# Performance work log

Hardware: AMD Instinct MI355X
Metric: run time of the kernel (lower is better)

The kernel has to match this reference:

```python
import jax, jax.numpy as jnp
import numpy as np
import math

B, S, D, H = 2, 2048, 1024, 16
DK = D // H  # 64


def _rope_tables(seq_len, dim):
    # matches RotaryEmbedding: inv_freq over arange(0, dim, 2)/dim
    inv_freq = 1.0 / (10000.0 ** (jnp.arange(0, dim, 2, dtype=jnp.float32) / dim))
    pos = jnp.arange(seq_len, dtype=jnp.float32)
    freqs = pos[:, None] * inv_freq[None, :]  # [S, dim/2]
    return jnp.cos(freqs), jnp.sin(freqs)


def _apply_rope(x, cos, sin):
    # x: [B, S, H, DK]; cos/sin: [S, DK/2] -> broadcast over heads
    cos = cos[:, None, :]
    sin = sin[:, None, :]
    t = x.shape[-1] // 2
    x1, x2 = x[..., :t], x[..., t:]
    return jnp.concatenate([x1 * cos - x2 * sin, x1 * sin + x2 * cos], axis=-1)


def setup_inputs() -> dict:
    key = jax.random.key(0)
    ks = jax.random.split(key, 12)
    sc = 1.0 / math.sqrt(D)
    inp = {
        'q': jax.random.normal(ks[0], (B, S, D), jnp.float32),
        'k': jax.random.normal(ks[1], (B, S, D), jnp.float32),
        'v': jax.random.normal(ks[2], (B, S, D), jnp.float32),
        'mask': jnp.tril(jnp.ones((S, S), jnp.int32))[None, None, :, :],  # causal [1,1,S,S]
        'Wq': jax.random.normal(ks[3], (D, D), jnp.float32) * sc,
        'bq': jnp.zeros((D,), jnp.float32),
        'Wk': jax.random.normal(ks[4], (D, D), jnp.float32) * sc,
        'bk': jnp.zeros((D,), jnp.float32),
        'Wv': jax.random.normal(ks[5], (D, D), jnp.float32) * sc,
        'bv': jnp.zeros((D,), jnp.float32),
        'Wo': jax.random.normal(ks[6], (D, D), jnp.float32) * sc,
        'bo': jnp.zeros((D,), jnp.float32),
    }
    return inp


def reference(q, k, v, mask, Wq, bq, Wk, bk, Wv, bv, Wo, bo):
    b, sq, _ = q.shape
    sk = k.shape[1]
    # QKV projections (torch Linear: x @ W^T + b), split heads
    qh = (q @ Wq.T + bq).reshape(b, sq, H, DK)
    kh = (k @ Wk.T + bk).reshape(b, sk, H, DK)
    vh = (v @ Wv.T + bv).reshape(b, sk, H, DK)
    # RoPE on q and k
    cos_q, sin_q = _rope_tables(sq, DK)
    cos_k, sin_k = _rope_tables(sk, DK)
    qh = _apply_rope(qh, cos_q, sin_q)
    kh = _apply_rope(kh, cos_k, sin_k)
    # masked softmax attention: [B,H,Sq,Sk]
    scores = jnp.einsum('bqhd,bkhd->bhqk', qh, kh) / math.sqrt(DK)
    scores = jnp.where(mask == 0, jnp.float32(-10000.0), scores)
    attn = jax.nn.softmax(scores, axis=-1)
    out = jnp.einsum('bhqk,bkhd->bqhd', attn, vh).reshape(b, sq, D)
    return out @ Wo.T + bo
```

## Files before the change

kernel.cpp:

```cpp
#include <hip/hip_runtime.h>
#include <math.h>

#define BB  2
#define SS  2048
#define DD  1024
#define HH  16
#define DKK 64

typedef __attribute__((ext_vector_type(8))) short bfrag;
typedef __attribute__((ext_vector_type(4))) float f32x4;

__device__ __forceinline__ unsigned short f2bf(float x) {
    union { float f; unsigned u; } v; v.f = x;
    unsigned r = v.u + 0x7FFF + ((v.u >> 16) & 1);
    return (unsigned short)(r >> 16);
}
__device__ __forceinline__ void async16(const void* g, void* l) {
    __builtin_amdgcn_global_load_lds(
        (const __attribute__((address_space(1))) void*)g,
        (__attribute__((address_space(3))) void*)l, 16, 0, 0);
}

__global__ __launch_bounds__(256)
void cvt_all(const float* __restrict__ q, const float* __restrict__ k,
             const float* __restrict__ v, const float* __restrict__ wq,
             const float* __restrict__ wk, const float* __restrict__ wv,
             const float* __restrict__ wo, unsigned short* __restrict__ ws)
{
    int b = blockIdx.x;
    const float* src; unsigned short* dst;
    const size_t MI = 1048576;
    if      (b <  4096) { src = q;  dst = ws;           }
    else if (b <  8192) { src = k;  dst = ws + 4*MI;  b -= 4096;  }
    else if (b < 12288) { src = v;  dst = ws + 8*MI;  b -= 8192;  }
    else if (b < 13312) { src = wq; dst = ws + 12*MI; b -= 12288; }
    else if (b < 14336) { src = wk; dst = ws + 13*MI; b -= 13312; }
    else if (b < 15360) { src = wv; dst = ws + 14*MI; b -= 14336; }
    else                { src = wo; dst = ws + 15*MI; b -= 15360; }
    size_t off = (size_t)b * 1024 + threadIdx.x * 4;
    float4 x = *(const float4*)(src + off);
    ushort4 o;
    o.x = f2bf(x.x); o.y = f2bf(x.y); o.z = f2bf(x.z); o.w = f2bf(x.w);
    *(ushort4*)(dst + off) = o;
}

__global__ __launch_bounds__(256, 3)
void gemm_qkv(const unsigned short* __restrict__ qA, const unsigned short* __restrict__ kA,
              const unsigned short* __restrict__ vA, const unsigned short* __restrict__ Wqb,
              const unsigned short* __restrict__ Wkb, const unsigned short* __restrict__ Wvb,
              const float* __restrict__ bq, const float* __restrict__ bk,
              const float* __restrict__ bv,
              unsigned short* __restrict__ qo, unsigned short* __restrict__ ko,
              unsigned short* __restrict__ vo)
{
    __shared__ unsigned short As[128 * 32];
    __shared__ unsigned short Bs[128 * 32];

    const int wsel = blockIdx.z;
    const unsigned short* A = (wsel == 0) ? qA : (wsel == 1) ? kA : vA;
    const unsigned short* W = (wsel == 0) ? Wqb : (wsel == 1) ? Wkb : Wvb;
    const float* bias       = (wsel == 0) ? bq : (wsel == 1) ? bk : bv;
    unsigned short* outp    = (wsel == 0) ? qo : (wsel == 1) ? ko : vo;

    const int t = threadIdx.x, w = t >> 6, lane = t & 63;
    const int lq = lane & 15, quad = lane >> 4;
    const int m0 = blockIdx.y * 128, n0 = blockIdx.x * 128;
    const int wm = (w >> 1) * 64, wn = (w & 1) * 64;
    const int srow = lane >> 2, sch = lane & 3;

    f32x4 acc[4][4] = {};

    for (int kt = 0; kt < 32; ++kt) {
        const int kofs = kt * 32;
        #pragma unroll
        for (int p = 0; p < 2; ++p) {
            const int rb = (p * 4 + w) * 16;
            async16(A + (size_t)(m0 + rb + srow) * 1024 + kofs + sch * 8,
                    (char*)As + (p * 4 + w) * 1024);
            async16(W + (size_t)(n0 + rb + srow) * 1024 + kofs + sch * 8,
                    (char*)Bs + (p * 4 + w) * 1024);
        }
        __syncthreads();
        bfrag a[4], b[4];
        #pragma unroll
        for (int i = 0; i < 4; ++i)
            a[i] = *(const bfrag*)&As[(wm + i * 16 + lq) * 32 + quad * 8];
        #pragma unroll
        for (int j = 0; j < 4; ++j)
            b[j] = *(const bfrag*)&Bs[(wn + j * 16 + lq) * 32 + quad * 8];
        #pragma unroll
        for (int i = 0; i < 4; ++i)
            #pragma unroll
            for (int j = 0; j < 4; ++j)
                acc[i][j] = __builtin_amdgcn_mfma_f32_16x16x32_bf16(a[i], b[j], acc[i][j], 0, 0, 0);
        __syncthreads();
    }

    if (wsel == 2) {
        #pragma unroll
        for (int j = 0; j < 4; ++j) {
            const int n = n0 + wn + j * 16 + lq;
            const int hh = n >> 6, d = n & 63;
            const float bj = bias[n];
            #pragma unroll
            for (int i = 0; i < 4; ++i)
                #pragma unroll
                for (int r = 0; r < 4; ++r) {
                    const int m = m0 + wm + i * 16 + quad * 4 + r;
                    const int bb2 = m >> 11, s = m & (SS - 1);
                    outp[(((size_t)(bb2 * HH + hh)) * SS + s) * DKK + d] = f2bf(acc[i][j][r] + bj);
                }
        }
    } else {
        const float osc = (wsel == 0) ? 0.18033688011112042f : 1.0f;
        #pragma unroll
        for (int jc = 0; jc < 2; ++jc) {
            const int n1 = n0 + wn + jc * 16 + lq;
            const float b1 = bias[n1], b2 = bias[n1 + 32];
            const int ifq = jc * 16 + lq;
            const int hh = n1 >> 6;
            const float inv_rev = exp2f(-(float)ifq * 0.4152410118609203f) * 0.15915494309189535f;
            #pragma unroll
            for (int i = 0; i < 4; ++i)
                #pragma unroll
                for (int r = 0; r < 4; ++r) {
                    const int m = m0 + wm + i * 16 + quad * 4 + r;
                    const int bb2 = m >> 11, s = m & (SS - 1);
                    float rev = (float)s * inv_rev;
                    rev -= floorf(rev);
                    const float sn = __builtin_amdgcn_sinf(rev);
                    const float cs = __builtin_amdgcn_cosf(rev);
                    const float va = acc[i][jc][r] + b1;
                    const float vb = acc[i][jc + 2][r] + b2;
                    const size_t base = (((size_t)(bb2 * HH + hh)) * SS + s) * DKK;
                    outp[base + ifq]      = f2bf((va * cs - vb * sn) * osc);
                    outp[base + ifq + 32] = f2bf((va * sn + vb * cs) * osc);
                }
        }
    }
}

__global__ __launch_bounds__(256)
void transpose_v(const unsigned short* __restrict__ vh, unsigned short* __restrict__ vt)
{
    __shared__ unsigned short T[64 * 64];
    const int t = threadIdx.x;
    const int s0 = blockIdx.x * 64;
    const int bh = blockIdx.y;
    const size_t base = (size_t)bh * SS * DKK;

    #pragma unroll
    for (int p = 0; p < 2; ++p) {
        const int idx = p * 256 + t;
        const int srow = idx >> 3, ch = idx & 7;
        uint4 dta = *(const uint4*)(vh + base + (size_t)(s0 + srow) * DKK + ch * 8);
        const unsigned short* e = (const unsigned short*)&dta;
        #pragma unroll
        for (int jj = 0; jj < 8; ++jj) {
            const int d = ch * 8 + jj;
            const int sw = ((d ^ (d >> 3)) & 7) << 3;
            T[d * 64 + (srow ^ sw)] = e[jj];
        }
    }
    __syncthreads();
    #pragma unroll
    for (int p = 0; p < 2; ++p) {
        const int idx = p * 256 + t;
        const int d = idx >> 3, c = idx & 7;
        const int sw = ((d ^ (d >> 3)) & 7) << 3;
        uint4 dta = *(const uint4*)&T[d * 64 + ((c * 8) ^ sw)];
        *(uint4*)(vt + base + (size_t)d * SS + s0 + c * 8) = dta;
    }
}

__global__ __launch_bounds__(256, 4)
void attn_mfma(const unsigned short* __restrict__ qh,
               const unsigned short* __restrict__ kh,
               const unsigned short* __restrict__ vt,
               unsigned short* __restrict__ ao)
{
    __shared__ unsigned short Ks[2 * 64 * 32];
    __shared__ unsigned short Vt[2 * 64 * 32];
    __shared__ unsigned short Ps[64 * 72];

    const int t = threadIdx.x, w = t >> 6, lane = t & 63;
    const int lq = lane & 15, quad = lane >> 4;
    const int srow = lane >> 2, sch = lane & 3;
    const int bh = blockIdx.y;
    const int base16 = (blockIdx.x + (bh & 15)) & 31;
    const int qtx = (bh < 16) ? base16 : 31 - base16;
    const int q0 = qtx * 64;
    const size_t bhq = (size_t)bh * SS * DKK;

    bfrag qb[2];
    #pragma unroll
    for (int h = 0; h < 2; ++h)
        qb[h] = *(const bfrag*)(qh + bhq +
            (size_t)(q0 + w * 16 + lq) * 64 + h * 32 + quad * 8);

    f32x4 o[4] = {};
    float mst = -1e30f, lst = 0.f;
    const int qmaxw = q0 + w * 16 + 15;

    for (int kt = 0; kt <= qtx; ++kt) {
        const int k0 = kt * 64;
        __syncthreads();
        #pragma unroll
        for (int h = 0; h < 2; ++h) {
            async16(kh + bhq + (size_t)(k0 + w * 16 + srow) * 64 + h * 32 + sch * 8,
                    (char*)&Ks[h * 64 * 32 + w * 16 * 32]);
            async16(vt + bhq + (size_t)(w * 16 + srow) * SS + k0 + h * 32 + sch * 8,
                    (char*)&Vt[h * 64 * 32 + w * 16 * 32]);
        }
        __syncthreads();

        if (k0 <= qmaxw) {
            f32x4 sc[4] = {};
            #pragma unroll
            for (int j = 0; j < 4; ++j) {
                bfrag kb0 = *(const bfrag*)&Ks[(j * 16 + lq) * 32 + quad * 8];
                bfrag kb1 = *(const bfrag*)&Ks[64 * 32 + (j * 16 + lq) * 32 + quad * 8];
                sc[j] = __builtin_amdgcn_mfma_f32_16x16x32_bf16(kb0, qb[0], sc[j], 0, 0, 0);
                sc[j] = __builtin_amdgcn_mfma_f32_16x16x32_bf16(kb1, qb[1], sc[j], 0, 0, 0);
            }
            if (kt == qtx) {
                const int qg = q0 + w * 16 + lq;
                #pragma unroll
                for (int j = 0; j < 4; ++j)
                    #pragma unroll
                    for (int r = 0; r < 4; ++r) {
                        const int kg = k0 + j * 16 + quad * 4 + r;
                        if (kg > qg) sc[j][r] = -1e30f;
                    }
            }

            float mx = -1e30f;
            #pragma unroll
            for (int j = 0; j < 4; ++j)
                #pragma unroll
                for (int r = 0; r < 4; ++r) mx = fmaxf(mx, sc[j][r]);
            mx = fmaxf(mx, __shfl_xor(mx, 16));
            mx = fmaxf(mx, __shfl_xor(mx, 32));
            const float mn = fmaxf(mst, mx);
            const float al = exp2f(mst - mn);
            float rs = 0.f;
            #pragma unroll
            for (int j = 0; j < 4; ++j)
                #pragma unroll
                for (int r = 0; r < 4; ++r) {
                    const float p = exp2f(sc[j][r] - mn);
                    sc[j][r] = p; rs += p;
                }
            rs += __shfl_xor(rs, 16);
            rs += __shfl_xor(rs, 32);
            lst = lst * al + rs;
            mst = mn;
            #pragma unroll
            for (int rr = 0; rr < 4; ++rr) {
                const float a = __shfl(al, quad * 4 + rr);
                #pragma unroll
                for (int j2 = 0; j2 < 4; ++j2) o[j2][rr] *= a;
            }
            #pragma unroll
            for (int j = 0; j < 4; ++j) {
                ushort4 pk;
                pk.x = f2bf(sc[j][0]); pk.y = f2bf(sc[j][1]);
                pk.z = f2bf(sc[j][2]); pk.w = f2bf(sc[j][3]);
                *(ushort4*)&Ps[(w * 16 + lq) * 72 + j * 16 + quad * 4] = pk;
            }

            bfrag pa0 = *(const bfrag*)&Ps[(w * 16 + lq) * 72 + quad * 8];
            bfrag pa1 = *(const bfrag*)&Ps[(w * 16 + lq) * 72 + 32 + quad * 8];
            #pragma unroll
            for (int j2 = 0; j2 < 4; ++j2) {
                bfrag vb0 = *(const bfrag*)&Vt[(j2 * 16 + lq) * 32 + quad * 8];
                bfrag vb1 = *(const bfrag*)&Vt[64 * 32 + (j2 * 16 + lq) * 32 + quad * 8];
                o[j2] = __builtin_amdgcn_mfma_f32_16x16x32_bf16(pa0, vb0, o[j2], 0, 0, 0);
                o[j2] = __builtin_amdgcn_mfma_f32_16x16x32_bf16(pa1, vb1, o[j2], 0, 0, 0);
            }
        }
    }

    const int b = bh >> 4, hh = bh & 15;
    #pragma unroll
    for (int r = 0; r < 4; ++r) {
        const float li = __shfl(lst, quad * 4 + r);
        const float inv = 1.0f / li;
        const int s = q0 + w * 16 + quad * 4 + r;
        const size_t rowb = ((size_t)(b * SS + s)) * DD + hh * DKK;
        #pragma unroll
        for (int j2 = 0; j2 < 4; ++j2)
            ao[rowb + j2 * 16 + lq] = f2bf(o[j2][r] * inv);
    }
}

__global__ __launch_bounds__(256, 2)
void gemm_o(const unsigned short* __restrict__ A, const unsigned short* __restrict__ W,
            const float* __restrict__ bias, float* __restrict__ out)
{
    __shared__ unsigned short As[64 * 32];
    __shared__ unsigned short Bs[128 * 32];

    const int t = threadIdx.x, w = t >> 6, lane = t & 63;
    const int lq = lane & 15, quad = lane >> 4;
    const int m0 = blockIdx.y * 64, n0 = blockIdx.x * 128;
    const int wm = (w >> 1) * 32, wn = (w & 1) * 64;
    const int srow = lane >> 2, sch = lane & 3;

    f32x4 acc[2][4] = {};

    for (int kt = 0; kt < 32; ++kt) {
        const int kofs = kt * 32;
        async16(A + (size_t)(m0 + w * 16 + srow) * 1024 + kofs + sch * 8,
                (char*)As + w * 1024);
        #pragma unroll
        for (int p = 0; p < 2; ++p) {
            const int rb = (p * 4 + w) * 16;
            async16(W + (size_t)(n0 + rb + srow) * 1024 + kofs + sch * 8,
                    (char*)Bs + (p * 4 + w) * 1024);
        }
        __syncthreads();
        bfrag a[2], b[4];
        #pragma unroll
        for (int i = 0; i < 2; ++i)
            a[i] = *(const bfrag*)&As[(wm + i * 16 + lq) * 32 + quad * 8];
        #pragma unroll
        for (int j = 0; j < 4; ++j)
            b[j] = *(const bfrag*)&Bs[(wn + j * 16 + lq) * 32 + quad * 8];
        #pragma unroll
        for (int i = 0; i < 2; ++i)
            #pragma unroll
            for (int j = 0; j < 4; ++j)
                acc[i][j] = __builtin_amdgcn_mfma_f32_16x16x32_bf16(a[i], b[j], acc[i][j], 0, 0, 0);
        __syncthreads();
    }

    #pragma unroll
    for (int j = 0; j < 4; ++j) {
        const int n = n0 + wn + j * 16 + lq;
        const float bj = bias[n];
        #pragma unroll
        for (int i = 0; i < 2; ++i)
            #pragma unroll
            for (int r = 0; r < 4; ++r) {
                const int m = m0 + wm + i * 16 + quad * 4 + r;
                out[(size_t)m * DD + n] = acc[i][j][r] + bj;
            }
    }
}

extern "C" void kernel_launch(void* const* d_in, const int* in_sizes, int n_in,
                              void* d_out, int out_size, void* d_ws, size_t ws_size,
                              hipStream_t stream)
{
    const float* q  = (const float*)d_in[0];
    const float* k  = (const float*)d_in[1];
    const float* v  = (const float*)d_in[2];
    const float* Wq = (const float*)d_in[4];
    const float* bq = (const float*)d_in[5];
    const float* Wk = (const float*)d_in[6];
    const float* bk = (const float*)d_in[7];
    const float* Wv = (const float*)d_in[8];
    const float* bv = (const float*)d_in[9];
    const float* Wo = (const float*)d_in[10];
    const float* bo = (const float*)d_in[11];
    float* out = (float*)d_out;

    unsigned short* ws = (unsigned short*)d_ws;
    const size_t MI = 1048576;
    unsigned short* qbf = ws;
    unsigned short* kbf = ws + 4 * MI;
    unsigned short* vbf = ws + 8 * MI;
    unsigned short* Wqb = ws + 12 * MI;
    unsigned short* Wkb = ws + 13 * MI;
    unsigned short* Wvb = ws + 14 * MI;
    unsigned short* Wob = ws + 15 * MI;
    unsigned short* qhp = ws + 16 * MI;
    unsigned short* khp = ws + 20 * MI;
    unsigned short* vhp = ws + 24 * MI;
    unsigned short* vtp = ws + 8 * MI;
    unsigned short* aop = ws + 28 * MI;

    const dim3 blk(256);

    cvt_all<<<dim3(16384), blk, 0, stream>>>(q, k, v, Wq, Wk, Wv, Wo, ws);

    gemm_qkv<<<dim3(8, 32, 3), blk, 0, stream>>>(qbf, kbf, vbf, Wqb, Wkb, Wvb,
                                                 bq, bk, bv, qhp, khp, vhp);

    transpose_v<<<dim3(32, 32), blk, 0, stream>>>(vhp, vtp);

    attn_mfma<<<dim3(32, 32), blk, 0, stream>>>(qhp, khp, vtp, aop);

    gemm_o<<<dim3(8, 64), blk, 0, stream>>>(aop, Wob, bo, out);
}
```

Measured before the change: 251.9 us.

## Split long causal attention tiles, fuse V transpose into projection, retile output GEMM

The V projection epilogue now writes V directly in transposed [bh][d][s] layout with packed stores, so the separate transpose kernel is dropped. Attention work is load-balanced with constant tables that map blocks to query tiles and key ranges. Query tiles 16..31 are split into two key halves whose partial O, max and sum values go to workspace, and a new combine kernel merges them. The output GEMM uses 64x64 tiles with higher occupancy to launch more blocks, at the cost of an extra kernel launch and partial-result traffic.

After: 237.8 us. 5.6% less time.

```diff
diff --git a/kernel.cpp b/kernel.cpp
--- a/kernel.cpp
+++ b/kernel.cpp
@@ -20,6 +20,28 @@
         (const __attribute__((address_space(1))) void*)g,
         (__attribute__((address_space(3))) void*)l, 16, 0, 0);
 }
+
+__constant__ int JQT[48] = {
+ 15,14,30,27,25,30,22,26,
+ 31,29,28,28,26,12,23,20,
+ 31,29,13,27,25,23,11,21,
+ 16,19,20,10,24,24,21, 9,
+ 16,17,18,17, 8, 6,22,18,
+  0, 1, 2, 3, 4, 5, 7,19};
+__constant__ int JKLO[48] = {
+  0, 0, 0, 0, 0,15,11,13,
+  0, 0,14, 0, 0, 0,12,10,
+ 16,15, 0,14,13, 0, 0,11,
+  8, 0, 0, 0,12, 0, 0, 0,
+  0, 0, 0, 9, 0, 0, 0, 9,
+  0, 0, 0, 0, 0, 0, 0,10};
+__constant__ int JPART[48] = {
+ 0,0,1,1,1,2,2,2,
+ 1,1,2,1,1,0,2,2,
+ 2,2,0,2,2,1,0,2,
+ 2,1,1,0,2,1,1,0,
+ 1,1,1,2,0,0,1,2,
+ 0,0,0,0,0,0,0,2};
 
 __global__ __launch_bounds__(256)
 void cvt_all(const float* __restrict__ q, const float* __restrict__ k,
@@ -103,13 +125,14 @@
             const int hh = n >> 6, d = n & 63;
             const float bj = bias[n];
             #pragma unroll
-            for (int i = 0; i < 4; ++i)
-                #pragma unroll
-                for (int r = 0; r < 4; ++r) {
-                    const int m = m0 + wm + i * 16 + quad * 4 + r;
-                    const int bb2 = m >> 11, s = m & (SS - 1);
-                    outp[(((size_t)(bb2 * HH + hh)) * SS + s) * DKK + d] = f2bf(acc[i][j][r] + bj);
-                }
+            for (int i = 0; i < 4; ++i) {
+                const int m = m0 + wm + i * 16 + quad * 4;
+                const int bb2 = m >> 11, sb = m & (SS - 1);
+                ushort4 pk;
+                pk.x = f2bf(acc[i][j][0] + bj); pk.y = f2bf(acc[i][j][1] + bj);
+                pk.z = f2bf(acc[i][j][2] + bj); pk.w = f2bf(acc[i][j][3] + bj);
+                *(ushort4*)(outp + ((size_t)((bb2 * HH + hh) * DKK + d)) * SS + sb) = pk;
+            }
         }
     } else {
         const float osc = (wsel == 0) ? 0.18033688011112042f : 1.0f;
@@ -140,44 +163,12 @@
     }
 }
 
-__global__ __launch_bounds__(256)
-void transpose_v(const unsigned short* __restrict__ vh, unsigned short* __restrict__ vt)
-{
-    __shared__ unsigned short T[64 * 64];
-    const int t = threadIdx.x;
-    const int s0 = blockIdx.x * 64;
-    const int bh = blockIdx.y;
-    const size_t base = (size_t)bh * SS * DKK;
-
-    #pragma unroll
-    for (int p = 0; p < 2; ++p) {
-        const int idx = p * 256 + t;
-        const int srow = idx >> 3, ch = idx & 7;
-        uint4 dta = *(const uint4*)(vh + base + (size_t)(s0 + srow) * DKK + ch * 8);
-        const unsigned short* e = (const unsigned short*)&dta;
-        #pragma unroll
-        for (int jj = 0; jj < 8; ++jj) {
-            const int d = ch * 8 + jj;
-            const int sw = ((d ^ (d >> 3)) & 7) << 3;
-            T[d * 64 + (srow ^ sw)] = e[jj];
-        }
-    }
-    __syncthreads();
-    #pragma unroll
-    for (int p = 0; p < 2; ++p) {
-        const int idx = p * 256 + t;
-        const int d = idx >> 3, c = idx & 7;
-        const int sw = ((d ^ (d >> 3)) & 7) << 3;
-        uint4 dta = *(const uint4*)&T[d * 64 + ((c * 8) ^ sw)];
-        *(uint4*)(vt + base + (size_t)d * SS + s0 + c * 8) = dta;
-    }
-}
-
-__global__ __launch_bounds__(256, 4)
+__global__ __launch_bounds__(256, 6)
 void attn_mfma(const unsigned short* __restrict__ qh,
                const unsigned short* __restrict__ kh,
                const unsigned short* __restrict__ vt,
-               unsigned short* __restrict__ ao)
+               unsigned short* __restrict__ ao,
+               float* __restrict__ pO, float* __restrict__ pml)
 {
     __shared__ unsigned short Ks[2 * 64 * 32];
     __shared__ unsigned short Vt[2 * 64 * 32];
@@ -186,9 +177,14 @@
     const int t = threadIdx.x, w = t >> 6, lane = t & 63;
     const int lq = lane & 15, quad = lane >> 4;
     const int srow = lane >> 2, sch = lane & 3;
-    const int bh = blockIdx.y;
-    const int base16 = (blockIdx.x + (bh & 15)) & 31;
-    const int qtx = (bh < 16) ? base16 : 31 - base16;
+
+    const int g  = blockIdx.x + 256 * blockIdx.y;
+    const int bh = g & 31;
+    const int w5 = g >> 5;
+    const int qtx  = JQT[w5];
+    const int klo  = JKLO[w5];
+    const int part = JPART[w5];
+    const int kthi = (part == 1) ? (((qtx + 1) >> 1) - 1) : qtx;
     const int q0 = qtx * 64;
     const size_t bhq = (size_t)bh * SS * DKK;
 
@@ -200,9 +196,8 @@
 
     f32x4 o[4] = {};
     float mst = -1e30f, lst = 0.f;
-    const int qmaxw = q0 + w * 16 + 15;
-
-    for (int kt = 0; kt <= qtx; ++kt) {
+
+    for (int kt = klo; kt <= kthi; ++kt) {
         const int k0 = kt * 64;
         __syncthreads();
         #pragma unroll
@@ -214,129 +209,173 @@
         }
         __syncthreads();
 
-        if (k0 <= qmaxw) {
-            f32x4 sc[4] = {};
-            #pragma unroll
-            for (int j = 0; j < 4; ++j) {
-                bfrag kb0 = *(const bfrag*)&Ks[(j * 16 + lq) * 32 + quad * 8];
-                bfrag kb1 = *(const bfrag*)&Ks[64 * 32 + (j * 16 + lq) * 32 + quad * 8];
-                sc[j] = __builtin_amdgcn_mfma_f32_16x16x32_bf16(kb0, qb[0], sc[j], 0, 0, 0);
-                sc[j] = __builtin_amdgcn_mfma_f32_16x16x32_bf16(kb1, qb[1], sc[j], 0, 0, 0);
-            }
-            if (kt == qtx) {
-                const int qg = q0 + w * 16 + lq;
-                #pragma unroll
-                for (int j = 0; j < 4; ++j)
-                    #pragma unroll
-                    for (int r = 0; r < 4; ++r) {
-                        const int kg = k0 + j * 16 + quad * 4 + r;
-                        if (kg > qg) sc[j][r] = -1e30f;
-                    }
-            }
-
-            float mx = -1e30f;
-            #pragma unroll
-            for (int j = 0; j < 4; ++j)
-                #pragma unroll
-                for (int r = 0; r < 4; ++r) mx = fmaxf(mx, sc[j][r]);
-            mx = fmaxf(mx, __shfl_xor(mx, 16));
-            mx = fmaxf(mx, __shfl_xor(mx, 32));
-            const float mn = fmaxf(mst, mx);
-            const float al = exp2f(mst - mn);
-            float rs = 0.f;
+        f32x4 sc[4] = {};
+        #pragma unroll
+        for (int j = 0; j < 4; ++j) {
+            bfrag kb0 = *(const bfrag*)&Ks[(j * 16 + lq) * 32 + quad * 8];
+            bfrag kb1 = *(const bfrag*)&Ks[64 * 32 + (j * 16 + lq) * 32 + quad * 8];
+            sc[j] = __builtin_amdgcn_mfma_f32_16x16x32_bf16(kb0, qb[0], sc[j], 0, 0, 0);
+            sc[j] = __builtin_amdgcn_mfma_f32_16x16x32_bf16(kb1, qb[1], sc[j], 0, 0, 0);
+        }
+        if (kt == qtx) {
+            const int qg = q0 + w * 16 + lq;
             #pragma unroll
             for (int j = 0; j < 4; ++j)
                 #pragma unroll
                 for (int r = 0; r < 4; ++r) {
-                    const float p = exp2f(sc[j][r] - mn);
-                    sc[j][r] = p; rs += p;
+                    const int kg = k0 + j * 16 + quad * 4 + r;
+                    if (kg > qg) sc[j][r] = -1e30f;
                 }
-            rs += __shfl_xor(rs, 16);
-            rs += __shfl_xor(rs, 32);
-            lst = lst * al + rs;
-            mst = mn;
-            #pragma unroll
-            for (int rr = 0; rr < 4; ++rr) {
-                const float a = __shfl(al, quad * 4 + rr);
-                #pragma unroll
-                for (int j2 = 0; j2 < 4; ++j2) o[j2][rr] *= a;
+        }
+
+        float mx = -1e30f;
+        #pragma unroll
+        for (int j = 0; j < 4; ++j)
+            #pragma unroll
+            for (int r = 0; r < 4; ++r) mx = fmaxf(mx, sc[j][r]);
+        mx = fmaxf(mx, __shfl_xor(mx, 16));
+        mx = fmaxf(mx, __shfl_xor(mx, 32));
+        const float mn = fmaxf(mst, mx);
+        const float al = exp2f(mst - mn);
+        float rs = 0.f;
+        #pragma unroll
+        for (int j = 0; j < 4; ++j)
+            #pragma unroll
+            for (int r = 0; r < 4; ++r) {
+                const float p = exp2f(sc[j][r] - mn);
+                sc[j][r] = p; rs += p;
             }
-            #pragma unroll
-            for (int j = 0; j < 4; ++j) {
-                ushort4 pk;
-                pk.x = f2bf(sc[j][0]); pk.y = f2bf(sc[j][1]);
-                pk.z = f2bf(sc[j][2]); pk.w = f2bf(sc[j][3]);
-                *(ushort4*)&Ps[(w * 16 + lq) * 72 + j * 16 + quad * 4] = pk;
-            }
-
-            bfrag pa0 = *(const bfrag*)&Ps[(w * 16 + lq) * 72 + quad * 8];
-            bfrag pa1 = *(const bfrag*)&Ps[(w * 16 + lq) * 72 + 32 + quad * 8];
-            #pragma unroll
-            for (int j2 = 0; j2 < 4; ++j2) {
-                bfrag vb0 = *(const bfrag*)&Vt[(j2 * 16 + lq) * 32 + quad * 8];
-                bfrag vb1 = *(const bfrag*)&Vt[64 * 32 + (j2 * 16 + lq) * 32 + quad * 8];
-                o[j2] = __builtin_amdgcn_mfma_f32_16x16x32_bf16(pa0, vb0, o[j2], 0, 0, 0);
-                o[j2] = __builtin_amdgcn_mfma_f32_16x16x32_bf16(pa1, vb1, o[j2], 0, 0, 0);
-            }
-        }
-    }
-
-    const int b = bh >> 4, hh = bh & 15;
+        rs += __shfl_xor(rs, 16);
+        rs += __shfl_xor(rs, 32);
+        lst = lst * al + rs;
+        mst = mn;
+        #pragma unroll
+        for (int rr = 0; rr < 4; ++rr) {
+            const float a = __shfl(al, quad * 4 + rr);
+            #pragma unroll
+            for (int j2 = 0; j2 < 4; ++j2) o[j2][rr] *= a;
+        }
+        #pragma unroll
+        for (int j = 0; j < 4; ++j) {
+            ushort4 pk;
+            pk.x = f2bf(sc[j][0]); pk.y = f2bf(sc[j][1]);
+            pk.z = f2bf(sc[j][2]); pk.w = f2bf(sc[j][3]);
+            *(ushort4*)&Ps[(w * 16 + lq) * 72 + j * 16 + quad * 4] = pk;
+        }
+
+        bfrag pa0 = *(const bfrag*)&Ps[(w * 16 + lq) * 72 + quad * 8];
+        bfrag pa1 = *(const bfrag*)&Ps[(w * 16 + lq) * 72 + 32 + quad * 8];
+        #pragma unroll
+        for (int j2 = 0; j2 < 4; ++j2) {
+            bfrag vb0 = *(const bfrag*)&Vt[(j2 * 16 + lq) * 32 + quad * 8];
+            bfrag vb1 = *(const bfrag*)&Vt[64 * 32 + (j2 * 16 + lq) * 32 + quad * 8];
+            o[j2] = __builtin_amdgcn_mfma_f32_16x16x32_bf16(pa0, vb0, o[j2], 0, 0, 0);
+            o[j2] = __builtin_amdgcn_mfma_f32_16x16x32_bf16(pa1, vb1, o[j2], 0, 0, 0);
+        }
+    }
+
+    if (part == 0) {
+        const int b = bh >> 4, hh = bh & 15;
+        #pragma unroll
+        for (int r = 0; r < 4; ++r) {
+            const float li = __shfl(lst, quad * 4 + r);
+            const float inv = 1.0f / li;
+            const int s = q0 + w * 16 + quad * 4 + r;
+            const size_t rowb = ((size_t)(b * SS + s)) * DD + hh * DKK;
+            #pragma unroll
+            for (int j2 = 0; j2 < 4; ++j2)
+                ao[rowb + j2 * 16 + lq] = f2bf(o[j2][r] * inv);
+        }
+    } else {
+        const int pidx = (bh * 16 + (qtx - 16)) * 2 + (part - 1);
+        float* po = pO + (size_t)pidx * 4096;
+        if (quad == 0) {
+            pml[pidx * 128 + w * 16 + lq]      = mst;
+            pml[pidx * 128 + 64 + w * 16 + lq] = lst;
+        }
+        #pragma unroll
+        for (int r = 0; r < 4; ++r)
+            #pragma unroll
+            for (int j2 = 0; j2 < 4; ++j2)
+                po[(w * 16 + quad * 4 + r) * 64 + j2 * 16 + lq] = o[j2][r];
+    }
+}
+
+__global__ __launch_bounds__(256)
+void combine(const float* __restrict__ pO, const float* __restrict__ pml,
+             unsigned short* __restrict__ ao)
+{
+    const int ti = blockIdx.x, bh = blockIdx.y;
+    const int qtx = 16 + ti;
+    const int p0 = (bh * 16 + ti) * 2;
+    const float* O1 = pO + (size_t)p0 * 4096;
+    const float* O2 = O1 + 4096;
+    const float* ml1 = pml + p0 * 128;
+    const float* ml2 = ml1 + 128;
+
+    const int t = threadIdx.x;
+    const int row = t >> 2, c0 = (t & 3) * 16;
+    const float m1 = ml1[row], l1 = ml1[64 + row];
+    const float m2 = ml2[row], l2 = ml2[64 + row];
+    const float mm = fmaxf(m1, m2);
+    const float w1 = exp2f(m1 - mm), w2 = exp2f(m2 - mm);
+    const float inv = 1.0f / (w1 * l1 + w2 * l2);
+
+    const int b = bh >> 4, h = bh & 15;
+    const int s = qtx * 64 + row;
+    const size_t ob = ((size_t)(b * SS + s)) * DD + h * DKK + c0;
     #pragma unroll
-    for (int r = 0; r < 4; ++r) {
-        const float li = __shfl(lst, quad * 4 + r);
-        const float inv = 1.0f / li;
-        const int s = q0 + w * 16 + quad * 4 + r;
-        const size_t rowb = ((size_t)(b * SS + s)) * DD + hh * DKK;
-        #pragma unroll
-        for (int j2 = 0; j2 < 4; ++j2)
-            ao[rowb + j2 * 16 + lq] = f2bf(o[j2][r] * inv);
-    }
-}
-
-__global__ __launch_bounds__(256, 2)
+    for (int c = 0; c < 16; c += 4) {
+        float4 a = *(const float4*)(O1 + row * 64 + c0 + c);
+        float4 d = *(const float4*)(O2 + row * 64 + c0 + c);
+        ushort4 u;
+        u.x = f2bf((a.x * w1 + d.x * w2) * inv);
+        u.y = f2bf((a.y * w1 + d.y * w2) * inv);
+        u.z = f2bf((a.z * w1 + d.z * w2) * inv);
+        u.w = f2bf((a.w * w1 + d.w * w2) * inv);
+        *(ushort4*)(ao + ob + c) = u;
+    }
+}
+
+__global__ __launch_bounds__(256, 4)
 void gemm_o(const unsigned short* __restrict__ A, const unsigned short* __restrict__ W,
             const float* __restrict__ bias, float* __restrict__ out)
 {
     __shared__ unsigned short As[64 * 32];
-    __shared__ unsigned short Bs[128 * 32];
+    __shared__ unsigned short Bs[64 * 32];
 
     const int t = threadIdx.x, w = t >> 6, lane = t & 63;
     const int lq = lane & 15, quad = lane >> 4;
-    const int m0 = blockIdx.y * 64, n0 = blockIdx.x * 128;
-    const int wm = (w >> 1) * 32, wn = (w & 1) * 64;
+    const int m0 = blockIdx.y * 64, n0 = blockIdx.x * 64;
+    const int wm = (w >> 1) * 32, wn = (w & 1) * 32;
     const int srow = lane >> 2, sch = lane & 3;
 
-    f32x4 acc[2][4] = {};
+    f32x4 acc[2][2] = {};
 
     for (int kt = 0; kt < 32; ++kt) {
         const int kofs = kt * 32;
         async16(A + (size_t)(m0 + w * 16 + srow) * 1024 + kofs + sch * 8,
                 (char*)As + w * 1024);
-        #pragma unroll
-        for (int p = 0; p < 2; ++p) {
-            const int rb = (p * 4 + w) * 16;
-            async16(W + (size_t)(n0 + rb + srow) * 1024 + kofs + sch * 8,
-                    (char*)Bs + (p * 4 + w) * 1024);
-        }
-        __syncthreads();
-        bfrag a[2], b[4];
+        async16(W + (size_t)(n0 + w * 16 + srow) * 1024 + kofs + sch * 8,
+                (char*)Bs + w * 1024);
+        __syncthreads();
+        bfrag a[2], b[2];
         #pragma unroll
         for (int i = 0; i < 2; ++i)
             a[i] = *(const bfrag*)&As[(wm + i * 16 + lq) * 32 + quad * 8];
         #pragma unroll
-        for (int j = 0; j < 4; ++j)
+        for (int j = 0; j < 2; ++j)
             b[j] = *(const bfrag*)&Bs[(wn + j * 16 + lq) * 32 + quad * 8];
         #pragma unroll
         for (int i = 0; i < 2; ++i)
             #pragma unroll
-            for (int j = 0; j < 4; ++j)
+            for (int j = 0; j < 2; ++j)
                 acc[i][j] = __builtin_amdgcn_mfma_f32_16x16x32_bf16(a[i], b[j], acc[i][j], 0, 0, 0);
         __syncthreads();
     }
 
     #pragma unroll
-    for (int j = 0; j < 4; ++j) {
+    for (int j = 0; j < 2; ++j) {
         const int n = n0 + wn + j * 16 + lq;
         const float bj = bias[n];
         #pragma unroll
@@ -377,20 +416,21 @@
     unsigned short* Wob = ws + 15 * MI;
     unsigned short* qhp = ws + 16 * MI;
     unsigned short* khp = ws + 20 * MI;
-    unsigned short* vhp = ws + 24 * MI;
-    unsigned short* vtp = ws + 8 * MI;
+    unsigned short* vtp = ws + 24 * MI;
     unsigned short* aop = ws + 28 * MI;
+    float* pO  = (float*)ws;
+    float* pml = (float*)(ws + 12 * MI);
 
     const dim3 blk(256);
 
     cvt_all<<<dim3(16384), blk, 0, stream>>>(q, k, v, Wq, Wk, Wv, Wo, ws);
 
     gemm_qkv<<<dim3(8, 32, 3), blk, 0, stream>>>(qbf, kbf, vbf, Wqb, Wkb, Wvb,
-                                                 bq, bk, bv, qhp, khp, vhp);
-
-    transpose_v<<<dim3(32, 32), blk, 0, stream>>>(vhp, vtp);
-
-    attn_mfma<<<dim3(32, 32), blk, 0, stream>>>(qhp, khp, vtp, aop);
-
-    gemm_o<<<dim3(8, 64), blk, 0, stream>>>(aop, Wob, bo, out);
-}
+                                                 bq, bk, bv, qhp, khp, vtp);
+
+    attn_mfma<<<dim3(256, 6), blk, 0, stream>>>(qhp, khp, vtp, aop, pO, pml);
+
+    combine<<<dim3(16, 32), blk, 0, stream>>>(pO, pml, aop);
+
+    gemm_o<<<dim3(16, 64), blk, 0, stream>>>(aop, Wob, bo, out);
+}
```
